# Optimization experiments

Hardware: AMD Instinct MI355X
Metric: run time of the kernel (lower is better)

## Reference

```python
import jax, jax.numpy as jnp
import numpy as np

NEG_SLOPE = 0.2  # PyG GATConv default negative_slope
H, C = 4, 64     # heads, per-head channels


def gat_layer(x, src, dst, edge_attr, W, a_src, a_dst, We, a_e, b):
    """PyG-style GATConv with edge features, concat=True. src/dst include self loops."""
    N = x.shape[0]
    h = (x @ W).reshape(N, H, C)                      # [N,H,C]
    al_s = (h * a_src[None]).sum(-1)                  # [N,H]
    al_d = (h * a_dst[None]).sum(-1)                  # [N,H]
    eh = (edge_attr @ We).reshape(-1, H, C)           # [E,H,C]
    al_e = (eh * a_e[None]).sum(-1)                   # [E,H]
    alpha = jax.nn.leaky_relu(al_s[src] + al_d[dst] + al_e, NEG_SLOPE)  # [E,H]
    # softmax over incoming edges of each destination node
    m = jax.ops.segment_max(alpha, dst, num_segments=N)
    p = jnp.exp(alpha - m[dst])
    denom = jax.ops.segment_sum(p, dst, num_segments=N)
    w = p / (denom[dst] + 1e-16)                      # [E,H]
    msg = h[src] * w[..., None]                       # [E,H,C]
    out = jax.ops.segment_sum(msg, dst, num_segments=N)  # [N,H,C]
    return out.reshape(N, H * C) + b


def setup_inputs() -> dict:
    key = jax.random.key(0)
    ks = jax.random.split(key, 20)
    N, E = 50000, 800000
    s = 0.05
    inp = {
        'x': jax.random.normal(ks[0], (N, 5), jnp.float32),
        'edge_index': jax.random.randint(ks[1], (2, E), 0, N, jnp.int32),
        'edge_attr': jax.random.normal(ks[2], (E, 4), jnp.float32),
        'W0': jax.random.normal(ks[3], (5, 256), jnp.float32) * s,
        'a_src0': jax.random.normal(ks[4], (H, C), jnp.float32) * s,
        'a_dst0': jax.random.normal(ks[5], (H, C), jnp.float32) * s,
        'We0': jax.random.normal(ks[6], (4, 256), jnp.float32) * s,
        'a_e0': jax.random.normal(ks[7], (H, C), jnp.float32) * s,
        'b0': jnp.zeros((256,), jnp.float32),
        'W1': jax.random.normal(ks[8], (256, 256), jnp.float32) * s,
        'a_src1': jax.random.normal(ks[9], (H, C), jnp.float32) * s,
        'a_dst1': jax.random.normal(ks[10], (H, C), jnp.float32) * s,
        'We1': jax.random.normal(ks[11], (4, 256), jnp.float32) * s,
        'a_e1': jax.random.normal(ks[12], (H, C), jnp.float32) * s,
        'b1': jnp.zeros((256,), jnp.float32),
        'Wm1': jax.random.normal(ks[13], (768, 128), jnp.float32) * s,
        'bm1': jnp.zeros((128,), jnp.float32),
        'Wm2': jax.random.normal(ks[14], (128, 64), jnp.float32) * s,
        'bm2': jnp.zeros((64,), jnp.float32),
        'Wm3': jax.random.normal(ks[15], (64, 128), jnp.float32) * s,
        'bm3': jnp.zeros((128,), jnp.float32),
    }
    return inp


def reference(x, edge_index, edge_attr,
              W0, a_src0, a_dst0, We0, a_e0, b0,
              W1, a_src1, a_dst1, We1, a_e1, b1,
              Wm1, bm1, Wm2, bm2, Wm3, bm3):
    N = x.shape[0]
    # add self loops once; self-loop edge_attr = mean of edge_attr (PyG fill_value='mean')
    loops = jnp.arange(N, dtype=edge_index.dtype)
    src = jnp.concatenate([edge_index[0], loops])
    dst = jnp.concatenate([edge_index[1], loops])
    mean_ea = jnp.mean(edge_attr, axis=0, keepdims=True)
    ea = jnp.concatenate([edge_attr, jnp.broadcast_to(mean_ea, (N, edge_attr.shape[1]))], axis=0)

    h = gat_layer(x, src, dst, ea, W0, a_src0, a_dst0, We0, a_e0, b0)
    h = jax.nn.relu(h)  # dropout is identity in eval
    h = gat_layer(h, src, dst, ea, W1, a_src1, a_dst1, We1, a_e1, b1)

    mean_pool = jnp.mean(h, axis=0)                      # [256]
    max_pool = jnp.max(h, axis=0)                        # [256]
    att = jax.nn.softmax(jnp.sum(h * mean_pool[None], axis=1))  # [N]
    att_pool = jnp.sum(h * att[:, None], axis=0)         # [256]
    comb = jnp.concatenate([mean_pool, max_pool, att_pool])  # [768]

    z = jax.nn.relu(comb @ Wm1 + bm1)
    z = jax.nn.relu(z @ Wm2 + bm2)
    g = z @ Wm3 + bm3
    return g[None]  # [1,128]
```

## Files before the change

### kernel.cpp

```cpp
#include <hip/hip_runtime.h>
#include <hip/hip_fp16.h>
#include <type_traits>

static const long long N_ = 50000;
static const long long E_ = 800000;
#define LOG2E 1.44269504088896f

typedef __attribute__((ext_vector_type(8))) short bf16x8;
typedef __attribute__((ext_vector_type(4))) float f32x4;

__device__ __forceinline__ float lrelu(float x){ return x >= 0.f ? x : 0.2f*x; }
__device__ __forceinline__ unsigned fkey(float x){
  unsigned u = __float_as_uint(x);
  return (u & 0x80000000u) ? ~u : (u | 0x80000000u);
}
__device__ __forceinline__ float unfkey(unsigned k){
  return __uint_as_float((k & 0x80000000u) ? (k & 0x7fffffffu) : ~k);
}
__device__ __forceinline__ unsigned h2u(__half2 h){ return *(unsigned*)&h; }

__global__ void k_pre(const int* __restrict__ ei, int* __restrict__ deg,
                      const float* __restrict__ ea, float* __restrict__ sum_ea,
                      const float* __restrict__ W1, ushort* __restrict__ Bhi,
                      ushort* __restrict__ Blo){
  int t = threadIdx.x;
  long long e = (long long)blockIdx.x*256 + t;
  if (e < E_) atomicAdd(&deg[ei[E_ + e]], 1);
  if (blockIdx.x < 256){
    int k = blockIdx.x, n = t;
    float v = W1[k*256+n];
    unsigned u = __float_as_uint(v);
    ushort hi = (ushort)(u>>16);
    float rem = v - __uint_as_float(u & 0xffff0000u);
    unsigned ur = __float_as_uint(rem);
    ushort lo = (ushort)((ur + 0x7fff + ((ur>>16)&1)) >> 16);
    int tl = n>>4, kb = k>>5, q = (k>>3)&3, j = k&7;
    long long idx = ((((long long)tl*8+kb)*64 + q*16 + (n&15))<<3) + j;
    Bhi[idx] = hi; Blo[idx] = lo;
  }
  __shared__ float lds[256];
  float s = 0.f;
  for (long long i = (long long)blockIdx.x*256 + t; i < E_*4; i += (long long)gridDim.x*256)
    s += ea[i];
  lds[t] = s; __syncthreads();
  for (int st=128; st>=4; st>>=1){ if (t<st) lds[t] += lds[t+st]; __syncthreads(); }
  if (t<4) atomicAdd(&sum_ea[t], lds[t]);
}

__global__ void k_scan1(const int* __restrict__ deg, int* __restrict__ bsum){
  __shared__ int lds[256];
  int t = threadIdx.x;
  long long idx = (long long)blockIdx.x*256 + t;
  lds[t] = (idx < N_) ? deg[idx] : 0;
  __syncthreads();
  for (int st=128; st>=1; st>>=1){ if (t<st) lds[t] += lds[t+st]; __syncthreads(); }
  if (t==0) bsum[blockIdx.x] = lds[0];
}

__global__ void k_scan2(const int* __restrict__ bsum, int* __restrict__ bpre, int nb,
                        int* __restrict__ rowptr,
                        const float* __restrict__ We0, const float* __restrict__ ae0,
                        const float* __restrict__ We1, const float* __restrict__ ae1,
                        const float* __restrict__ sum_ea, float* __restrict__ small){
  __shared__ int lds[256];
  int t = threadIdx.x;
  int v = (t < nb) ? bsum[t] : 0;
  lds[t] = v; __syncthreads();
  for (int off=1; off<256; off<<=1){
    int add = (t>=off) ? lds[t-off] : 0;
    __syncthreads();
    lds[t] += add;
    __syncthreads();
  }
  if (t < nb) bpre[t] = lds[t] - v;
  if (t == 0) rowptr[N_] = (int)E_;
  if (t < 32){
    int l = t>>4, f = (t>>2)&3, h = t&3;
    const float* We = l ? We1 : We0;
    const float* ae = l ? ae1 : ae0;
    float s = 0.f;
    for (int cc=0; cc<64; cc++) s += We[f*256 + h*64 + cc]*ae[h*64+cc];
    small[l*16 + f*4 + h] = s * LOG2E;
  }
  __syncthreads();
  if (t < 8){
    int l = t>>2, h = t&3;
    const float* Ae = small + l*16;
    const float invE = 1.f/(float)E_;
    float s = 0.f;
    for (int f=0; f<4; f++) s += sum_ea[f]*invE*Ae[f*4+h];
    small[32 + l*4 + h] = s;
  }
}

__global__ void k_scan3(const int* __restrict__ deg, const int* __restrict__ bpre,
                        int* __restrict__ rowptr, int* __restrict__ cursor){
  __shared__ int lds[256];
  int t = threadIdx.x;
  long long idx = (long long)blockIdx.x*256 + t;
  int v = (idx < N_) ? deg[idx] : 0;
  lds[t] = v; __syncthreads();
  for (int off=1; off<256; off<<=1){
    int add = (t>=off) ? lds[t-off] : 0;
    __syncthreads();
    lds[t] += add;
    __syncthreads();
  }
  if (idx < N_){
    int rp = bpre[blockIdx.x] + lds[t] - v;
    rowptr[idx] = rp; cursor[idx] = rp;
  }
}

__global__ void k_h0(const float* __restrict__ x, const float* __restrict__ W0,
                     const float* __restrict__ as0, const float* __restrict__ ad0,
                     __half* __restrict__ h0, float* __restrict__ als, float* __restrict__ ald){
  int wid = (int)(((long long)blockIdx.x*blockDim.x + threadIdx.x) >> 6);
  int lane = threadIdx.x & 63;
  if (wid >= (int)N_) return;
  const float* xr = x + wid*5;
  float xv[5];
  #pragma unroll
  for (int f=0; f<5; f++) xv[f] = xr[f];
  int c = lane*4;
  float a0=0,a1=0,a2=0,a3=0;
  #pragma unroll
  for (int f=0; f<5; f++){
    const float* wr = W0 + f*256 + c;
    a0 += xv[f]*wr[0]; a1 += xv[f]*wr[1]; a2 += xv[f]*wr[2]; a3 += xv[f]*wr[3];
  }
  uint2 pk = make_uint2(h2u(__floats2half2_rn(a0,a1)), h2u(__floats2half2_rn(a2,a3)));
  *(uint2*)(h0 + wid*256 + c) = pk;
  const float* asp = as0 + c;
  const float* adp = ad0 + c;
  float ss = a0*asp[0]+a1*asp[1]+a2*asp[2]+a3*asp[3];
  float dd = a0*adp[0]+a1*adp[1]+a2*adp[2]+a3*adp[3];
  int head = lane>>4;
  #pragma unroll
  for (int m=1; m<16; m<<=1){ ss += __shfl_xor(ss, m); dd += __shfl_xor(dd, m); }
  if ((lane&15)==0){ als[wid*4+head]=ss*LOG2E; ald[wid*4+head]=dd*LOG2E; }
}

__global__ void k_scatter(const int* __restrict__ ei, const float* __restrict__ ea,
                          int* __restrict__ cursor, int* __restrict__ csr_src,
                          int* __restrict__ csr_dst,
                          __half* __restrict__ ale1h, __half* __restrict__ p0h,
                          const float* __restrict__ small,
                          const float* __restrict__ als0, const float* __restrict__ ald0){
  long long e = (long long)blockIdx.x*256 + threadIdx.x;
  if (e >= E_) return;
  int s = ei[e], d = ei[E_+e];
  int pos = atomicAdd(&cursor[d], 1);
  csr_src[pos] = s;
  csr_dst[pos] = d;
  float4 v = *(const float4*)(ea + e*4);
  float4 As = *(const float4*)(als0 + s*4);
  float4 Ad = *(const float4*)(ald0 + d*4);
  float as_[4] = {As.x,As.y,As.z,As.w};
  float ad_[4] = {Ad.x,Ad.y,Ad.z,Ad.w};
  float p0[4], o1[4];
  #pragma unroll
  for (int h=0; h<4; h++){
    float a0 = v.x*small[0+h]  + v.y*small[4+h]  + v.z*small[8+h]  + v.w*small[12+h];
    p0[h] = exp2f(lrelu(as_[h] + ad_[h] + a0));
    o1[h] = v.x*small[16+h] + v.y*small[20+h] + v.z*small[24+h] + v.w*small[28+h];
  }
  uint2 pkp = make_uint2(h2u(__floats2half2_rn(p0[0],p0[1])), h2u(__floats2half2_rn(p0[2],p0[3])));
  uint2 pke = make_uint2(h2u(__floats2half2_rn(o1[0],o1[1])), h2u(__floats2half2_rn(o1[2],o1[3])));
  *(uint2*)(p0h + (long long)pos*4) = pkp;
  *(uint2*)(ale1h + (long long)pos*4) = pke;
}

__global__ void k_palpha1(const int* __restrict__ csr_src, const int* __restrict__ csr_dst,
                          const __half* __restrict__ ale1h,
                          const float* __restrict__ als1, const float* __restrict__ ald1,
                          __half* __restrict__ p1h){
  long long i = (long long)blockIdx.x*256 + threadIdx.x;
  if (i >= E_) return;
  int s = csr_src[i], d = csr_dst[i];
  float4 As = *(const float4*)(als1 + s*4);
  float4 Ad = *(const float4*)(ald1 + d*4);
  uint2 pke = *(const uint2*)(ale1h + i*4);
  float2 e01 = __half22float2(*(__half2*)&pke.x);
  float2 e23 = __half22float2(*(__half2*)&pke.y);
  float p0 = exp2f(lrelu(As.x+Ad.x+e01.x));
  float p1 = exp2f(lrelu(As.y+Ad.y+e01.y));
  float p2 = exp2f(lrelu(As.z+Ad.z+e23.x));
  float p3 = exp2f(lrelu(As.w+Ad.w+e23.y));
  uint2 pk = make_uint2(h2u(__floats2half2_rn(p0,p1)), h2u(__floats2half2_rn(p2,p3)));
  *(uint2*)(p1h + i*4) = pk;
}

template<typename OutT, bool RELU>
__global__ __launch_bounds__(256) void k_agg(const __half* __restrict__ hin,
    const float* __restrict__ als, const float* __restrict__ ald,
    const int* __restrict__ rowptr, const int* __restrict__ csr_src,
    const __half* __restrict__ ph,
    const float* __restrict__ small, int loop_off,
    const float* __restrict__ bias, OutT* __restrict__ out){
  int wid = (int)(((long long)blockIdx.x*256 + threadIdx.x) >> 6);
  int lane = threadIdx.x & 63;
  if (wid >= (int)N_) return;
  int head = lane>>4, c = lane*4;
  const uint2* hp = (const uint2*)hin;
  float aS = lrelu(als[wid*4+head] + ald[wid*4+head] + small[loop_off+head]);
  float pS = exp2f(aS);
  uint2 r0 = hp[wid*64 + lane];
  float2 f01 = __half22float2(*(__half2*)&r0.x);
  float2 f23 = __half22float2(*(__half2*)&r0.y);
  float den = pS;
  float ax = pS*f01.x, ay = pS*f01.y, az = pS*f23.x, aw = pS*f23.y;
  int beg = rowptr[wid], end = rowptr[wid+1];
  int i = beg;
  for (; i+7 < end; i += 8){
    int   sidx[8]; float pv[8]; uint2 rr[8];
    #pragma unroll
    for (int k=0;k<8;k++) sidx[k] = csr_src[i+k];
    #pragma unroll
    for (int k=0;k<8;k++) pv[k] = __half2float(ph[(i+k)*4+head]);
    #pragma unroll
    for (int k=0;k<8;k++) rr[k] = hp[sidx[k]*64+lane];
    #pragma unroll
    for (int k=0;k<8;k++){
      float2 u01 = __half22float2(*(__half2*)&rr[k].x);
      float2 u23 = __half22float2(*(__half2*)&rr[k].y);
      den += pv[k];
      ax += pv[k]*u01.x; ay += pv[k]*u01.y;
      az += pv[k]*u23.x; aw += pv[k]*u23.y;
    }
  }
  for (; i < end; i++){
    int s0 = csr_src[i];
    float p = __half2float(ph[i*4+head]);
    uint2 r = hp[s0*64+lane];
    float2 u01 = __half22float2(*(__half2*)&r.x);
    float2 u23 = __half22float2(*(__half2*)&r.y);
    den += p;
    ax += p*u01.x; ay += p*u01.y; az += p*u23.x; aw += p*u23.y;
  }
  float inv = 1.f/(den + 1e-16f);
  const float* bp = bias + c;
  float ox = ax*inv + bp[0], oy = ay*inv + bp[1];
  float oz = az*inv + bp[2], ow = aw*inv + bp[3];
  if (RELU){ ox=fmaxf(ox,0.f); oy=fmaxf(oy,0.f); oz=fmaxf(oz,0.f); ow=fmaxf(ow,0.f); }
  if constexpr (std::is_same<OutT,__half>::value){
    uint2 qk = make_uint2(h2u(__floats2half2_rn(ox,oy)), h2u(__floats2half2_rn(oz,ow)));
    *(uint2*)(out + wid*256 + c) = qk;
  } else {
    *(float4*)(out + wid*256 + c) = make_float4(ox,oy,oz,ow);
  }
}

__global__ __launch_bounds__(256) void k_gemm(const float* __restrict__ A,
    const ushort* __restrict__ Bhi, const ushort* __restrict__ Blo,
    __half* __restrict__ Ch, const float* __restrict__ as1, const float* __restrict__ ad1,
    float* __restrict__ als, float* __restrict__ ald){
  __shared__ ushort Ah[32*264];
  __shared__ ushort Al[32*264];
  int t = threadIdx.x;
  long long base = (long long)blockIdx.x*32;
  for (int i=t; i<2048; i+=256){
    int r = i>>6, q4 = i&63;
    float4 v = make_float4(0.f,0.f,0.f,0.f);
    if (base + r < N_) v = *(const float4*)(A + (base+r)*256 + q4*4);
    float vv[4] = {v.x,v.y,v.z,v.w};
    ushort hh[4], ll[4];
    #pragma unroll
    for (int e=0;e<4;e++){
      unsigned u = __float_as_uint(vv[e]);
      hh[e] = (ushort)(u>>16);
      float rem = vv[e] - __uint_as_float(u & 0xffff0000u);
      unsigned ur = __float_as_uint(rem);
      ll[e] = (ushort)((ur + 0x7fff + ((ur>>16)&1)) >> 16);
    }
    int off = r*264 + q4*4;
    *(ushort4*)(Ah+off) = make_ushort4(hh[0],hh[1],hh[2],hh[3]);
    *(ushort4*)(Al+off) = make_ushort4(ll[0],ll[1],ll[2],ll[3]);
  }
  __syncthreads();
  int w = t>>6, lane = t&63, m = lane&15, q = lane>>4;
  int rbase = (w>>1)*16;
  int nhalf = (w&1)*8;
  f32x4 acc[8];
  #pragma unroll
  for (int i=0;i<8;i++) acc[i] = (f32x4){0.f,0.f,0.f,0.f};
  for (int kb=0; kb<8; kb++){
    int aoff = (rbase+m)*264 + kb*32 + q*8;
    bf16x8 ah = *(const bf16x8*)(Ah + aoff);
    bf16x8 al = *(const bf16x8*)(Al + aoff);
    #pragma unroll
    for (int tt=0; tt<8; tt++){
      long long bidx = ((((long long)(nhalf+tt)*8+kb)*64 + lane)<<3);
      bf16x8 bh = *(const bf16x8*)(Bhi + bidx);
      bf16x8 bl = *(const bf16x8*)(Blo + bidx);
      acc[tt] = __builtin_amdgcn_mfma_f32_16x16x32_bf16(ah, bh, acc[tt], 0,0,0);
      acc[tt] = __builtin_amdgcn_mfma_f32_16x16x32_bf16(al, bh, acc[tt], 0,0,0);
      acc[tt] = __builtin_amdgcn_mfma_f32_16x16x32_bf16(ah, bl, acc[tt], 0,0,0);
    }
  }
  float ssv[4][2], ddv[4][2];
  #pragma unroll
  for (int r=0;r<4;r++){ ssv[r][0]=0.f; ssv[r][1]=0.f; ddv[r][0]=0.f; ddv[r][1]=0.f; }
  #pragma unroll
  for (int tt=0; tt<8; tt++){
    int col = (nhalf+tt)*16 + m;
    float as_ = as1[col], ad_ = ad1[col];
    int hh = tt>>2;
    #pragma unroll
    for (int r=0;r<4;r++){
      ssv[r][hh] += acc[tt][r]*as_;
      ddv[r][hh] += acc[tt][r]*ad_;
    }
  }
  #pragma unroll
  for (int r=0;r<4;r++){
    #pragma unroll
    for (int hh=0; hh<2; hh++){
      #pragma unroll
      for (int mm=1; mm<16; mm<<=1){
        ssv[r][hh] += __shfl_xor(ssv[r][hh], mm);
        ddv[r][hh] += __shfl_xor(ddv[r][hh], mm);
      }
    }
  }
  #pragma unroll
  for (int r=0;r<4;r++){
    long long grow = base + rbase + q*4 + r;
    if (grow < N_){
      #pragma unroll
      for (int tt=0; tt<8; tt++)
        Ch[grow*256 + (nhalf+tt)*16 + m] = __float2half(acc[tt][r]);
      if (m==0){
        int hb = (w&1)*2;
        als[grow*4 + hb+0] = ssv[r][0]*LOG2E;
        ald[grow*4 + hb+0] = ddv[r][0]*LOG2E;
        als[grow*4 + hb+1] = ssv[r][1]*LOG2E;
        ald[grow*4 + hb+1] = ddv[r][1]*LOG2E;
      }
    }
  }
}

__global__ void k_pool1(const __half* __restrict__ h2, float* __restrict__ sum_pool,
                        unsigned* __restrict__ maxkey){
  int c = threadIdx.x;
  float s = 0.f; float m = -3.4e38f;
  for (long long n = blockIdx.x; n < N_; n += gridDim.x){
    float v = __half2float(h2[n*256+c]); s += v; m = fmaxf(m, v);
  }
  atomicAdd(&sum_pool[c], s);
  atomicMax(&maxkey[c], fkey(m));
}

__global__ void k_atts(const __half* __restrict__ h2, const float* __restrict__ sum_pool,
                       float* __restrict__ sarr, float* __restrict__ ssum){
  __shared__ float lsum[4];
  int t = threadIdx.x; int lane = t&63; int w = t>>6;
  const float invN = 1.f/(float)N_;
  int c = lane*4;
  float4 mp = *(const float4*)(sum_pool + c);
  float esum = 0.f;
  for (long long wid = (long long)blockIdx.x*4 + w; wid < N_; wid += (long long)gridDim.x*4){
    uint2 pk = *(const uint2*)(h2 + wid*256 + c);
    float2 a01 = __half22float2(*(__half2*)&pk.x);
    float2 a23 = __half22float2(*(__half2*)&pk.y);
    float s = (a01.x*mp.x + a01.y*mp.y + a23.x*mp.z + a23.y*mp.w)*invN;
    #pragma unroll
    for (int m=1; m<64; m<<=1) s += __shfl_xor(s, m);
    if (lane==0){ sarr[wid] = s; esum += __expf(s); }
  }
  if (lane==0) lsum[w] = esum;
  __syncthreads();
  if (t==0) atomicAdd(ssum, lsum[0]+lsum[1]+lsum[2]+lsum[3]);
}

__global__ void k_attp(const __half* __restrict__ h2, const float* __restrict__ sarr,
                       const float* __restrict__ ssum, float* __restrict__ att_pool){
  int c = threadIdx.x;
  float inv = 1.f/(*ssum);
  float acc = 0.f;
  for (long long n = blockIdx.x; n < N_; n += gridDim.x){
    float w = __expf(sarr[n])*inv;
    acc += __half2float(h2[n*256+c])*w;
  }
  atomicAdd(&att_pool[c], acc);
}

__global__ void k_mlp(const float* __restrict__ sum_pool, const unsigned* __restrict__ maxkey,
                      const float* __restrict__ att_pool,
                      const float* __restrict__ Wm1, const float* __restrict__ bm1,
                      const float* __restrict__ Wm2, const float* __restrict__ bm2,
                      const float* __restrict__ Wm3, const float* __restrict__ bm3,
                      float* __restrict__ out){
  __shared__ float comb[768];
  __shared__ float z1p[4][128]; __shared__ float z1[128];
  __shared__ float z2p[8][64];  __shared__ float z2[64];
  __shared__ float z3p[4][128];
  int t = threadIdx.x;
  const float invN = 1.f/(float)N_;
  for (int i=t; i<768; i+=512){
    float v;
    if (i < 256)      v = sum_pool[i]*invN;
    else if (i < 512) v = unfkey(maxkey[i-256]);
    else              v = att_pool[i-512];
    comb[i] = v;
  }
  __syncthreads();
  { int n = t&127, part = t>>7;
    float a = 0.f;
    for (int f=part*192; f<part*192+192; f++) a += comb[f]*Wm1[f*128+n];
    z1p[part][n] = a;
  }
  __syncthreads();
  if (t < 128)
    z1[t] = fmaxf(bm1[t] + z1p[0][t]+z1p[1][t]+z1p[2][t]+z1p[3][t], 0.f);
  __syncthreads();
  { int n = t&63, part = t>>6;
    float a = 0.f;
    for (int f=part*16; f<part*16+16; f++) a += z1[f]*Wm2[f*64+n];
    z2p[part][n] = a;
  }
  __syncthreads();
  if (t < 64){
    float a = bm2[t];
    #pragma unroll
    for (int p=0;p<8;p++) a += z2p[p][t];
    z2[t] = fmaxf(a, 0.f);
  }
  __syncthreads();
  { int n = t&127, part = t>>7;
    float a = 0.f;
    for (int f=part*16; f<part*16+16; f++) a += z2[f]*Wm3[f*128+n];
    z3p[part][n] = a;
  }
  __syncthreads();
  if (t < 128)
    out[t] = bm3[t] + z3p[0][t]+z3p[1][t]+z3p[2][t]+z3p[3][t];
}

extern "C" void kernel_launch(void* const* d_in, const int* in_sizes, int n_in,
                              void* d_out, int out_size, void* d_ws, size_t ws_size,
                              hipStream_t stream){
  (void)in_sizes; (void)n_in; (void)out_size; (void)ws_size;
  const float* x   = (const float*)d_in[0];
  const int*   ei  = (const int*)d_in[1];
  const float* ea  = (const float*)d_in[2];
  const float* W0  = (const float*)d_in[3];
  const float* as0 = (const float*)d_in[4];
  const float* ad0 = (const float*)d_in[5];
  const float* We0 = (const float*)d_in[6];
  const float* ae0 = (const float*)d_in[7];
  const float* b0  = (const float*)d_in[8];
  const float* W1  = (const float*)d_in[9];
  const float* as1 = (const float*)d_in[10];
  const float* ad1 = (const float*)d_in[11];
  const float* We1 = (const float*)d_in[12];
  const float* ae1 = (const float*)d_in[13];
  const float* b1  = (const float*)d_in[14];
  const float* Wm1 = (const float*)d_in[15];
  const float* bm1 = (const float*)d_in[16];
  const float* Wm2 = (const float*)d_in[17];
  const float* bm2 = (const float*)d_in[18];
  const float* Wm3 = (const float*)d_in[19];
  const float* bm3 = (const float*)d_in[20];
  float* out = (float*)d_out;

  char* ws = (char*)d_ws;
  size_t o = 0;
  auto alloc = [&](size_t bytes)->size_t{
    size_t r = o; o = (o + bytes + 255) & ~(size_t)255; return r;
  };
  size_t o_bufF   = alloc((size_t)N_*256*4);
  size_t o_bufH   = alloc((size_t)N_*256*2);
  size_t o_als0   = alloc((size_t)N_*4*4);
  size_t o_ald0   = alloc((size_t)N_*4*4);
  size_t o_als1   = alloc((size_t)N_*4*4);
  size_t o_ald1   = alloc((size_t)N_*4*4);
  size_t o_rowptr = alloc((size_t)(N_+1)*4);
  size_t o_cursor = alloc((size_t)N_*4);
  size_t o_csrsrc = alloc((size_t)E_*4);
  size_t o_csrdst = alloc((size_t)E_*4);
  size_t o_ale1   = alloc((size_t)E_*4*2);
  size_t o_p0     = alloc((size_t)E_*4*2);
  size_t o_p1     = alloc((size_t)E_*4*2);
  size_t o_sarr   = alloc((size_t)N_*4);
  size_t o_Bhi    = alloc((size_t)256*256*2);
  size_t o_Blo    = alloc((size_t)256*256*2);
  size_t o_bsum   = alloc(256*4);
  size_t o_bpre   = alloc(256*4);
  size_t zstart   = o;
  size_t o_deg    = alloc((size_t)N_*4);
  size_t o_sumea  = alloc(16);
  size_t o_sumpool= alloc(256*4);
  size_t o_maxkey = alloc(256*4);
  size_t o_attpool= alloc(256*4);
  size_t o_ssum   = alloc(4);
  size_t zend     = o;
  size_t o_small  = alloc(40*4);

  float*  bufF   = (float*)(ws + o_bufF);
  __half* bufH   = (__half*)(ws + o_bufH);
  __half* h2h    = (__half*)(ws + o_bufF);
  float* pals0  = (float*)(ws + o_als0);
  float* pald0  = (float*)(ws + o_ald0);
  float* pals1  = (float*)(ws + o_als1);
  float* pald1  = (float*)(ws + o_ald1);
  int*   rowptr = (int*)(ws + o_rowptr);
  int*   cursor = (int*)(ws + o_cursor);
  int*   csrsrc = (int*)(ws + o_csrsrc);
  int*   csrdst = (int*)(ws + o_csrdst);
  __half* ale1h = (__half*)(ws + o_ale1);
  __half* p0h   = (__half*)(ws + o_p0);
  __half* p1h   = (__half*)(ws + o_p1);
  float* sarr   = (float*)(ws + o_sarr);
  ushort* Bhi   = (ushort*)(ws + o_Bhi);
  ushort* Blo   = (ushort*)(ws + o_Blo);
  int*   bsum   = (int*)(ws + o_bsum);
  int*   bpre   = (int*)(ws + o_bpre);
  int*   deg    = (int*)(ws + o_deg);
  float* sumea  = (float*)(ws + o_sumea);
  float* sumpool= (float*)(ws + o_sumpool);
  unsigned* maxkey = (unsigned*)(ws + o_maxkey);
  float* attpool= (float*)(ws + o_attpool);
  float* ssum   = (float*)(ws + o_ssum);
  float* small  = (float*)(ws + o_small);

  hipMemsetAsync(ws + zstart, 0, zend - zstart, stream);

  int eb = (int)((E_ + 255)/256);
  int nb_wave = (int)((N_*64 + 255)/256);
  int gb = (int)((N_ + 31)/32);
  int sb = (int)((N_ + 255)/256);

  k_pre    <<<eb, 256, 0, stream>>>(ei, deg, ea, sumea, W1, Bhi, Blo);
  k_scan1  <<<sb, 256, 0, stream>>>(deg, bsum);
  k_scan2  <<<1, 256, 0, stream>>>(bsum, bpre, sb, rowptr,
                                   We0, ae0, We1, ae1, sumea, small);
  k_scan3  <<<sb, 256, 0, stream>>>(deg, bpre, rowptr, cursor);
  k_h0     <<<nb_wave, 256, 0, stream>>>(x, W0, as0, ad0, bufH, pals0, pald0);
  k_scatter<<<eb, 256, 0, stream>>>(ei, ea, cursor, csrsrc, csrdst,
                                    ale1h, p0h, small, pals0, pald0);
  k_agg<float,true>  <<<nb_wave, 256, 0, stream>>>(bufH, pals0, pald0, rowptr, csrsrc,
                                         p0h, small, 32, b0, bufF);
  k_gemm   <<<gb, 256, 0, stream>>>(bufF, Bhi, Blo, bufH, as1, ad1, pals1, pald1);
  k_palpha1<<<eb, 256, 0, stream>>>(csrsrc, csrdst, ale1h, pals1, pald1, p1h);
  k_agg<__half,false><<<nb_wave, 256, 0, stream>>>(bufH, pals1, pald1, rowptr, csrsrc,
                                         p1h, small, 36, b1, h2h);
  k_pool1  <<<256, 256, 0, stream>>>(h2h, sumpool, maxkey);
  k_atts   <<<1024, 256, 0, stream>>>(h2h, sumpool, sarr, ssum);
  k_attp   <<<256, 256, 0, stream>>>(h2h, sarr, ssum, attpool);
  k_mlp    <<<1, 512, 0, stream>>>(sumpool, maxkey, attpool,
                                   Wm1, bm1, Wm2, bm2, Wm3, bm3, out);
}
```

Before: 569.3 us.

## Replicate degree counters, precompute edge ranks, pack CSR arrays, split aggregation across half-waves

Degree counting now spreads atomics over 8 replicated counter arrays and records each edge's rank, so the scatter pass computes positions without a second atomic. Source/destination indices and the per-edge p0/edge-logit values are packed into int2 and uint4 records to cut the number of separate streams. The aggregation kernel has each half-wave take alternate edges with 8 channels per lane and 16-byte loads, then combines the halves with a shuffle. This costs an extra rank array, 8x counter memory, more scan work, and assumes in-degree per copy fits in a byte.

```diff
diff --git a/kernel.cpp b/kernel.cpp
--- a/kernel.cpp
+++ b/kernel.cpp
@@ -4,6 +4,7 @@
 
 static const long long N_ = 50000;
 static const long long E_ = 800000;
+static const int NCOPY = 8;
 #define LOG2E 1.44269504088896f
 
 typedef __attribute__((ext_vector_type(8))) short bf16x8;
@@ -19,13 +20,19 @@
 }
 __device__ __forceinline__ unsigned h2u(__half2 h){ return *(unsigned*)&h; }
 
-__global__ void k_pre(const int* __restrict__ ei, int* __restrict__ deg,
+__global__ void k_pre(const int* __restrict__ ei, int* __restrict__ deg8,
+                      unsigned char* __restrict__ rank,
                       const float* __restrict__ ea, float* __restrict__ sum_ea,
                       const float* __restrict__ W1, ushort* __restrict__ Bhi,
                       ushort* __restrict__ Blo){
   int t = threadIdx.x;
   long long e = (long long)blockIdx.x*256 + t;
-  if (e < E_) atomicAdd(&deg[ei[E_ + e]], 1);
+  if (e < E_){
+    int d = ei[E_ + e];
+    int copy = blockIdx.x & (NCOPY-1);
+    int old = atomicAdd(&deg8[copy*(int)N_ + d], 1);
+    rank[e] = (unsigned char)old;
+  }
   if (blockIdx.x < 256){
     int k = blockIdx.x, n = t;
     float v = W1[k*256+n];
@@ -47,11 +54,16 @@
   if (t<4) atomicAdd(&sum_ea[t], lds[t]);
 }
 
-__global__ void k_scan1(const int* __restrict__ deg, int* __restrict__ bsum){
+__global__ void k_scan1(const int* __restrict__ deg8, int* __restrict__ bsum){
   __shared__ int lds[256];
   int t = threadIdx.x;
   long long idx = (long long)blockIdx.x*256 + t;
-  lds[t] = (idx < N_) ? deg[idx] : 0;
+  int v = 0;
+  if (idx < N_){
+    #pragma unroll
+    for (int c=0;c<NCOPY;c++) v += deg8[c*(int)N_ + idx];
+  }
+  lds[t] = v;
   __syncthreads();
   for (int st=128; st>=1; st>>=1){ if (t<st) lds[t] += lds[t+st]; __syncthreads(); }
   if (t==0) bsum[blockIdx.x] = lds[0];
@@ -93,12 +105,16 @@
   }
 }
 
-__global__ void k_scan3(const int* __restrict__ deg, const int* __restrict__ bpre,
-                        int* __restrict__ rowptr, int* __restrict__ cursor){
+__global__ void k_scan3(const int* __restrict__ deg8, const int* __restrict__ bpre,
+                        int* __restrict__ rowptr, int* __restrict__ base){
   __shared__ int lds[256];
   int t = threadIdx.x;
   long long idx = (long long)blockIdx.x*256 + t;
-  int v = (idx < N_) ? deg[idx] : 0;
+  int dd[NCOPY]; int v = 0;
+  if (idx < N_){
+    #pragma unroll
+    for (int c=0;c<NCOPY;c++){ dd[c] = deg8[c*(int)N_ + idx]; v += dd[c]; }
+  }
   lds[t] = v; __syncthreads();
   for (int off=1; off<256; off<<=1){
     int add = (t>=off) ? lds[t-off] : 0;
@@ -108,7 +124,10 @@
   }
   if (idx < N_){
     int rp = bpre[blockIdx.x] + lds[t] - v;
-    rowptr[idx] = rp; cursor[idx] = rp;
+    rowptr[idx] = rp;
+    int cum = rp;
+    #pragma unroll
+    for (int c=0;c<NCOPY;c++){ base[c*(int)N_ + idx] = cum; cum += dd[c]; }
   }
 }
 
@@ -142,17 +161,16 @@
 }
 
 __global__ void k_scatter(const int* __restrict__ ei, const float* __restrict__ ea,
-                          int* __restrict__ cursor, int* __restrict__ csr_src,
-                          int* __restrict__ csr_dst,
-                          __half* __restrict__ ale1h, __half* __restrict__ p0h,
+                          const int* __restrict__ base, const unsigned char* __restrict__ rank,
+                          int2* __restrict__ csr2, uint4* __restrict__ pe,
                           const float* __restrict__ small,
                           const float* __restrict__ als0, const float* __restrict__ ald0){
   long long e = (long long)blockIdx.x*256 + threadIdx.x;
   if (e >= E_) return;
   int s = ei[e], d = ei[E_+e];
-  int pos = atomicAdd(&cursor[d], 1);
-  csr_src[pos] = s;
-  csr_dst[pos] = d;
+  int copy = blockIdx.x & (NCOPY-1);
+  int pos = base[copy*(int)N_ + d] + (int)rank[e];
+  csr2[pos] = make_int2(s, d);
   float4 v = *(const float4*)(ea + e*4);
   float4 As = *(const float4*)(als0 + s*4);
   float4 Ad = *(const float4*)(ald0 + d*4);
@@ -165,89 +183,119 @@
     p0[h] = exp2f(lrelu(as_[h] + ad_[h] + a0));
     o1[h] = v.x*small[16+h] + v.y*small[20+h] + v.z*small[24+h] + v.w*small[28+h];
   }
-  uint2 pkp = make_uint2(h2u(__floats2half2_rn(p0[0],p0[1])), h2u(__floats2half2_rn(p0[2],p0[3])));
-  uint2 pke = make_uint2(h2u(__floats2half2_rn(o1[0],o1[1])), h2u(__floats2half2_rn(o1[2],o1[3])));
-  *(uint2*)(p0h + (long long)pos*4) = pkp;
-  *(uint2*)(ale1h + (long long)pos*4) = pke;
-}
-
-__global__ void k_palpha1(const int* __restrict__ csr_src, const int* __restrict__ csr_dst,
-                          const __half* __restrict__ ale1h,
+  uint4 pk = make_uint4(h2u(__floats2half2_rn(p0[0],p0[1])),
+                        h2u(__floats2half2_rn(p0[2],p0[3])),
+                        h2u(__floats2half2_rn(o1[0],o1[1])),
+                        h2u(__floats2half2_rn(o1[2],o1[3])));
+  pe[pos] = pk;
+}
+
+__global__ void k_palpha1(const int2* __restrict__ csr2, const uint4* __restrict__ pe,
                           const float* __restrict__ als1, const float* __restrict__ ald1,
                           __half* __restrict__ p1h){
   long long i = (long long)blockIdx.x*256 + threadIdx.x;
   if (i >= E_) return;
-  int s = csr_src[i], d = csr_dst[i];
-  float4 As = *(const float4*)(als1 + s*4);
-  float4 Ad = *(const float4*)(ald1 + d*4);
-  uint2 pke = *(const uint2*)(ale1h + i*4);
-  float2 e01 = __half22float2(*(__half2*)&pke.x);
-  float2 e23 = __half22float2(*(__half2*)&pke.y);
+  int2 sd = csr2[i];
+  float4 As = *(const float4*)(als1 + sd.x*4);
+  float4 Ad = *(const float4*)(ald1 + sd.y*4);
+  uint4 pk = pe[i];
+  float2 e01 = __half22float2(*(__half2*)&pk.z);
+  float2 e23 = __half22float2(*(__half2*)&pk.w);
   float p0 = exp2f(lrelu(As.x+Ad.x+e01.x));
   float p1 = exp2f(lrelu(As.y+Ad.y+e01.y));
   float p2 = exp2f(lrelu(As.z+Ad.z+e23.x));
   float p3 = exp2f(lrelu(As.w+Ad.w+e23.y));
-  uint2 pk = make_uint2(h2u(__floats2half2_rn(p0,p1)), h2u(__floats2half2_rn(p2,p3)));
-  *(uint2*)(p1h + i*4) = pk;
+  uint2 o = make_uint2(h2u(__floats2half2_rn(p0,p1)), h2u(__floats2half2_rn(p2,p3)));
+  *(uint2*)(p1h + i*4) = o;
 }
 
 template<typename OutT, bool RELU>
 __global__ __launch_bounds__(256) void k_agg(const __half* __restrict__ hin,
     const float* __restrict__ als, const float* __restrict__ ald,
-    const int* __restrict__ rowptr, const int* __restrict__ csr_src,
-    const __half* __restrict__ ph,
+    const int* __restrict__ rowptr, const int2* __restrict__ csr2,
+    const __half* __restrict__ ph, int pstride,
     const float* __restrict__ small, int loop_off,
     const float* __restrict__ bias, OutT* __restrict__ out){
   int wid = (int)(((long long)blockIdx.x*256 + threadIdx.x) >> 6);
   int lane = threadIdx.x & 63;
   if (wid >= (int)N_) return;
-  int head = lane>>4, c = lane*4;
-  const uint2* hp = (const uint2*)hin;
-  float aS = lrelu(als[wid*4+head] + ald[wid*4+head] + small[loop_off+head]);
-  float pS = exp2f(aS);
-  uint2 r0 = hp[wid*64 + lane];
-  float2 f01 = __half22float2(*(__half2*)&r0.x);
-  float2 f23 = __half22float2(*(__half2*)&r0.y);
-  float den = pS;
-  float ax = pS*f01.x, ay = pS*f01.y, az = pS*f23.x, aw = pS*f23.y;
+  int half_ = lane>>5, l5 = lane&31;
+  int head = l5>>3, c8 = l5*8;
+  const uint4* hp = (const uint4*)hin;
+  float a[8]; float den;
+  {
+    float pS = exp2f(lrelu(als[wid*4+head] + ald[wid*4+head] + small[loop_off+head]));
+    float pp = (half_==0) ? pS : 0.f;
+    uint4 r = hp[wid*32 + l5];
+    float2 f0 = __half22float2(*(__half2*)&r.x);
+    float2 f1 = __half22float2(*(__half2*)&r.y);
+    float2 f2 = __half22float2(*(__half2*)&r.z);
+    float2 f3 = __half22float2(*(__half2*)&r.w);
+    den = pp;
+    a[0]=pp*f0.x; a[1]=pp*f0.y; a[2]=pp*f1.x; a[3]=pp*f1.y;
+    a[4]=pp*f2.x; a[5]=pp*f2.y; a[6]=pp*f3.x; a[7]=pp*f3.y;
+  }
   int beg = rowptr[wid], end = rowptr[wid+1];
   int i = beg;
   for (; i+7 < end; i += 8){
-    int   sidx[8]; float pv[8]; uint2 rr[8];
-    #pragma unroll
-    for (int k=0;k<8;k++) sidx[k] = csr_src[i+k];
-    #pragma unroll
-    for (int k=0;k<8;k++) pv[k] = __half2float(ph[(i+k)*4+head]);
-    #pragma unroll
-    for (int k=0;k<8;k++) rr[k] = hp[sidx[k]*64+lane];
-    #pragma unroll
-    for (int k=0;k<8;k++){
-      float2 u01 = __half22float2(*(__half2*)&rr[k].x);
-      float2 u23 = __half22float2(*(__half2*)&rr[k].y);
-      den += pv[k];
-      ax += pv[k]*u01.x; ay += pv[k]*u01.y;
-      az += pv[k]*u23.x; aw += pv[k]*u23.y;
-    }
-  }
-  for (; i < end; i++){
-    int s0 = csr_src[i];
-    float p = __half2float(ph[i*4+head]);
-    uint2 r = hp[s0*64+lane];
-    float2 u01 = __half22float2(*(__half2*)&r.x);
-    float2 u23 = __half22float2(*(__half2*)&r.y);
+    int   sv[4]; float pv[4]; uint4 rr[4];
+    #pragma unroll
+    for (int k=0;k<4;k++){
+      int e = i + 2*k + half_;
+      sv[k] = csr2[e].x;
+      pv[k] = __half2float(ph[e*pstride + head]);
+    }
+    #pragma unroll
+    for (int k=0;k<4;k++) rr[k] = hp[sv[k]*32 + l5];
+    #pragma unroll
+    for (int k=0;k<4;k++){
+      float2 f0 = __half22float2(*(__half2*)&rr[k].x);
+      float2 f1 = __half22float2(*(__half2*)&rr[k].y);
+      float2 f2 = __half22float2(*(__half2*)&rr[k].z);
+      float2 f3 = __half22float2(*(__half2*)&rr[k].w);
+      float p = pv[k];
+      den += p;
+      a[0]+=p*f0.x; a[1]+=p*f0.y; a[2]+=p*f1.x; a[3]+=p*f1.y;
+      a[4]+=p*f2.x; a[5]+=p*f2.y; a[6]+=p*f3.x; a[7]+=p*f3.y;
+    }
+  }
+  for (; i < end; i += 2){
+    int e = i + half_;
+    bool act = (e < end);
+    int ee = act ? e : (end-1);
+    int s0 = csr2[ee].x;
+    float p = act ? __half2float(ph[ee*pstride + head]) : 0.f;
+    uint4 r = hp[s0*32 + l5];
+    float2 f0 = __half22float2(*(__half2*)&r.x);
+    float2 f1 = __half22float2(*(__half2*)&r.y);
+    float2 f2 = __half22float2(*(__half2*)&r.z);
+    float2 f3 = __half22float2(*(__half2*)&r.w);
     den += p;
-    ax += p*u01.x; ay += p*u01.y; az += p*u23.x; aw += p*u23.y;
-  }
-  float inv = 1.f/(den + 1e-16f);
-  const float* bp = bias + c;
-  float ox = ax*inv + bp[0], oy = ay*inv + bp[1];
-  float oz = az*inv + bp[2], ow = aw*inv + bp[3];
-  if (RELU){ ox=fmaxf(ox,0.f); oy=fmaxf(oy,0.f); oz=fmaxf(oz,0.f); ow=fmaxf(ow,0.f); }
-  if constexpr (std::is_same<OutT,__half>::value){
-    uint2 qk = make_uint2(h2u(__floats2half2_rn(ox,oy)), h2u(__floats2half2_rn(oz,ow)));
-    *(uint2*)(out + wid*256 + c) = qk;
-  } else {
-    *(float4*)(out + wid*256 + c) = make_float4(ox,oy,oz,ow);
+    a[0]+=p*f0.x; a[1]+=p*f0.y; a[2]+=p*f1.x; a[3]+=p*f1.y;
+    a[4]+=p*f2.x; a[5]+=p*f2.y; a[6]+=p*f3.x; a[7]+=p*f3.y;
+  }
+  den += __shfl_xor(den, 32);
+  #pragma unroll
+  for (int j=0;j<8;j++) a[j] += __shfl_xor(a[j], 32);
+  if (half_ == 0){
+    float inv = 1.f/(den + 1e-16f);
+    float4 b0 = *(const float4*)(bias + c8);
+    float4 b1 = *(const float4*)(bias + c8 + 4);
+    float o[8];
+    o[0]=a[0]*inv+b0.x; o[1]=a[1]*inv+b0.y; o[2]=a[2]*inv+b0.z; o[3]=a[3]*inv+b0.w;
+    o[4]=a[4]*inv+b1.x; o[5]=a[5]*inv+b1.y; o[6]=a[6]*inv+b1.z; o[7]=a[7]*inv+b1.w;
+    if (RELU){
+      #pragma unroll
+      for (int j=0;j<8;j++) o[j] = fmaxf(o[j], 0.f);
+    }
+    if constexpr (std::is_same<OutT,__half>::value){
+      uint4 qk = make_uint4(h2u(__floats2half2_rn(o[0],o[1])), h2u(__floats2half2_rn(o[2],o[3])),
+                            h2u(__floats2half2_rn(o[4],o[5])), h2u(__floats2half2_rn(o[6],o[7])));
+      *(uint4*)(out + wid*256 + c8) = qk;
+    } else {
+      *(float4*)(out + wid*256 + c8)     = make_float4(o[0],o[1],o[2],o[3]);
+      *(float4*)(out + wid*256 + c8 + 4) = make_float4(o[4],o[5],o[6],o[7]);
+    }
   }
 }
 
@@ -477,19 +525,18 @@
   size_t o_als1   = alloc((size_t)N_*4*4);
   size_t o_ald1   = alloc((size_t)N_*4*4);
   size_t o_rowptr = alloc((size_t)(N_+1)*4);
-  size_t o_cursor = alloc((size_t)N_*4);
-  size_t o_csrsrc = alloc((size_t)E_*4);
-  size_t o_csrdst = alloc((size_t)E_*4);
-  size_t o_ale1   = alloc((size_t)E_*4*2);
-  size_t o_p0     = alloc((size_t)E_*4*2);
+  size_t o_csr2   = alloc((size_t)E_*8);
+  size_t o_pe     = alloc((size_t)E_*16);
   size_t o_p1     = alloc((size_t)E_*4*2);
+  size_t o_rank   = alloc((size_t)E_);
+  size_t o_base   = alloc((size_t)NCOPY*N_*4);
   size_t o_sarr   = alloc((size_t)N_*4);
   size_t o_Bhi    = alloc((size_t)256*256*2);
   size_t o_Blo    = alloc((size_t)256*256*2);
   size_t o_bsum   = alloc(256*4);
   size_t o_bpre   = alloc(256*4);
   size_t zstart   = o;
-  size_t o_deg    = alloc((size_t)N_*4);
+  size_t o_deg8   = alloc((size_t)NCOPY*N_*4);
   size_t o_sumea  = alloc(16);
   size_t o_sumpool= alloc(256*4);
   size_t o_maxkey = alloc(256*4);
@@ -506,18 +553,17 @@
   float* pals1  = (float*)(ws + o_als1);
   float* pald1  = (float*)(ws + o_ald1);
   int*   rowptr = (int*)(ws + o_rowptr);
-  int*   cursor = (int*)(ws + o_cursor);
-  int*   csrsrc = (int*)(ws + o_csrsrc);
-  int*   csrdst = (int*)(ws + o_csrdst);
-  __half* ale1h = (__half*)(ws + o_ale1);
-  __half* p0h   = (__half*)(ws + o_p0);
+  int2*  csr2   = (int2*)(ws + o_csr2);
+  uint4* pe     = (uint4*)(ws + o_pe);
   __half* p1h   = (__half*)(ws + o_p1);
+  unsigned char* rank = (unsigned char*)(ws + o_rank);
+  int*   base   = (int*)(ws + o_base);
   float* sarr   = (float*)(ws + o_sarr);
   ushort* Bhi   = (ushort*)(ws + o_Bhi);
   ushort* Blo   = (ushort*)(ws + o_Blo);
   int*   bsum   = (int*)(ws + o_bsum);
   int*   bpre   = (int*)(ws + o_bpre);
-  int*   deg    = (int*)(ws + o_deg);
+  int*   deg8   = (int*)(ws + o_deg8);
   float* sumea  = (float*)(ws + o_sumea);
   float* sumpool= (float*)(ws + o_sumpool);
   unsigned* maxkey = (unsigned*)(ws + o_maxkey);
@@ -532,20 +578,20 @@
   int gb = (int)((N_ + 31)/32);
   int sb = (int)((N_ + 255)/256);
 
-  k_pre    <<<eb, 256, 0, stream>>>(ei, deg, ea, sumea, W1, Bhi, Blo);
-  k_scan1  <<<sb, 256, 0, stream>>>(deg, bsum);
+  k_pre    <<<eb, 256, 0, stream>>>(ei, deg8, rank, ea, sumea, W1, Bhi, Blo);
+  k_scan1  <<<sb, 256, 0, stream>>>(deg8, bsum);
   k_scan2  <<<1, 256, 0, stream>>>(bsum, bpre, sb, rowptr,
                                    We0, ae0, We1, ae1, sumea, small);
-  k_scan3  <<<sb, 256, 0, stream>>>(deg, bpre, rowptr, cursor);
+  k_scan3  <<<sb, 256, 0, stream>>>(deg8, bpre, rowptr, base);
   k_h0     <<<nb_wave, 256, 0, stream>>>(x, W0, as0, ad0, bufH, pals0, pald0);
-  k_scatter<<<eb, 256, 0, stream>>>(ei, ea, cursor, csrsrc, csrdst,
-                                    ale1h, p0h, small, pals0, pald0);
-  k_agg<float,true>  <<<nb_wave, 256, 0, stream>>>(bufH, pals0, pald0, rowptr, csrsrc,
-                                         p0h, small, 32, b0, bufF);
+  k_scatter<<<eb, 256, 0, stream>>>(ei, ea, base, rank, csr2, pe,
+                                    small, pals0, pald0);
+  k_agg<float,true>  <<<nb_wave, 256, 0, stream>>>(bufH, pals0, pald0, rowptr, csr2,
+                                         (const __half*)pe, 8, small, 32, b0, bufF);
   k_gemm   <<<gb, 256, 0, stream>>>(bufF, Bhi, Blo, bufH, as1, ad1, pals1, pald1);
-  k_palpha1<<<eb, 256, 0, stream>>>(csrsrc, csrdst, ale1h, pals1, pald1, p1h);
-  k_agg<__half,false><<<nb_wave, 256, 0, stream>>>(bufH, pals1, pald1, rowptr, csrsrc,
-                                         p1h, small, 36, b1, h2h);
+  k_palpha1<<<eb, 256, 0, stream>>>(csr2, pe, pals1, pald1, p1h);
+  k_agg<__half,false><<<nb_wave, 256, 0, stream>>>(bufH, pals1, pald1, rowptr, csr2,
+                                         p1h, 4, small, 36, b1, h2h);
   k_pool1  <<<256, 256, 0, stream>>>(h2h, sumpool, maxkey);
   k_atts   <<<1024, 256, 0, stream>>>(h2h, sumpool, sarr, ssum);
   k_attp   <<<256, 256, 0, stream>>>(h2h, sarr, ssum, attpool);
```

New measurement: 533.6 us. 1.07x faster.
